# Optimization experiments

Hardware: AMD Instinct MI355X
Metric: run time of the kernel (lower is better)

Reference implementation:

```python
import jax, jax.numpy as jnp
import numpy as np

N = 4096       # num nodes
E = 131072     # num edges (avg degree 32)
IN = 128       # in_channels
H = 256        # hidden_channels
NC = 16        # num_classes
NH = 4         # num_heads
HD = H // NH   # head dim
EPS = 1e-5


def setup_inputs() -> dict:
    key = jax.random.key(0)
    ks = jax.random.split(key, 16)
    p = lambda k, sh, s=0.05: jax.random.normal(k, sh, jnp.float32) * s
    return {
        "x": jax.random.normal(ks[0], (N, IN), jnp.float32),
        "edge_index": jax.random.randint(ks[1], (2, E), 0, N),
        "edge_attr": jax.random.uniform(ks[2], (E,), jnp.float32),
        # GCN layers
        "W_gcn1": p(ks[3], (IN, H)), "b_gcn1": jnp.zeros((H,), jnp.float32),
        "W_gcn2": p(ks[4], (H, H)), "b_gcn2": jnp.zeros((H,), jnp.float32),
        # Transformer encoder layer (post-norm, batch_first)
        "in_proj_w": p(ks[5], (3 * H, H)), "in_proj_b": jnp.zeros((3 * H,), jnp.float32),
        "out_proj_w": p(ks[6], (H, H)), "out_proj_b": jnp.zeros((H,), jnp.float32),
        "ln1_g": jnp.ones((H,), jnp.float32), "ln1_b": jnp.zeros((H,), jnp.float32),
        "ffn_w1": p(ks[7], (H, 4 * H)), "ffn_b1": jnp.zeros((4 * H,), jnp.float32),
        "ffn_w2": p(ks[8], (4 * H, H)), "ffn_b2": jnp.zeros((H,), jnp.float32),
        "ln2_g": jnp.ones((H,), jnp.float32), "ln2_b": jnp.zeros((H,), jnp.float32),
        # classifier head
        "W_cls": p(ks[9], (H, NC)), "b_cls": jnp.zeros((NC,), jnp.float32),
        # semantic decoder
        "W_d1": p(ks[10], (H, 2 * H)), "b_d1": jnp.zeros((2 * H,), jnp.float32),
        "W_d2": p(ks[11], (2 * H, 3)), "b_d2": jnp.zeros((3,), jnp.float32),
    }


def gcn_conv(x, edge_index, edge_weight, W, b):
    """PyG GCNConv: add self-loops, symmetric norm, gather-matmul-scatter."""
    n = x.shape[0]
    src, dst = edge_index[0], edge_index[1]
    loop = jnp.arange(n)
    src_f = jnp.concatenate([src, loop])
    dst_f = jnp.concatenate([dst, loop])
    ew_f = jnp.concatenate([edge_weight, jnp.ones((n,), x.dtype)])
    deg = jax.ops.segment_sum(ew_f, dst_f, num_segments=n)
    dinv = jnp.where(deg > 0, jax.lax.rsqrt(deg), 0.0)
    norm = dinv[src_f] * ew_f * dinv[dst_f]            # [E+N]
    h = x @ W                                          # [N,H]
    out = jax.ops.segment_sum(norm[:, None] * h[src_f], dst_f, num_segments=n)
    return out + b


def layer_norm(x, g, b):
    mu = jnp.mean(x, axis=-1, keepdims=True)
    var = jnp.mean(jnp.square(x - mu), axis=-1, keepdims=True)
    return (x - mu) * jax.lax.rsqrt(var + EPS) * g + b


def transformer_layer(x, in_proj_w, in_proj_b, out_proj_w, out_proj_b,
                      ln1_g, ln1_b, ffn_w1, ffn_b1, ffn_w2, ffn_b2, ln2_g, ln2_b):
    # Self-attention (seq = all N nodes, batch of 1), eval mode (no dropout)
    qkv = x @ in_proj_w.T + in_proj_b                  # [N,3H]
    q, k, v = jnp.split(qkv, 3, axis=-1)
    q = q.reshape(-1, NH, HD) * (1.0 / np.sqrt(HD))
    k = k.reshape(-1, NH, HD)
    v = v.reshape(-1, NH, HD)
    scores = jnp.einsum("nhd,mhd->hnm", q, k)          # [NH,N,N]
    attn = jax.nn.softmax(scores, axis=-1)
    ctx = jnp.einsum("hnm,mhd->nhd", attn, v).reshape(-1, H)
    attn_out = ctx @ out_proj_w.T + out_proj_b
    x = layer_norm(x + attn_out, ln1_g, ln1_b)         # post-norm
    ffn = jax.nn.relu(x @ ffn_w1 + ffn_b1) @ ffn_w2 + ffn_b2
    return layer_norm(x + ffn, ln2_g, ln2_b)


def reference(x, edge_index, edge_attr,
              W_gcn1, b_gcn1, W_gcn2, b_gcn2,
              in_proj_w, in_proj_b, out_proj_w, out_proj_b,
              ln1_g, ln1_b, ffn_w1, ffn_b1, ffn_w2, ffn_b2, ln2_g, ln2_b,
              W_cls, b_cls, W_d1, b_d1, W_d2, b_d2):
    x_local = jax.nn.relu(gcn_conv(x, edge_index, edge_attr, W_gcn1, b_gcn1))
    # F.dropout with training=False is identity
    x_local = gcn_conv(x_local, edge_index, edge_attr, W_gcn2, b_gcn2)
    x_global = transformer_layer(x_local, in_proj_w, in_proj_b, out_proj_w,
                                 out_proj_b, ln1_g, ln1_b, ffn_w1, ffn_b1,
                                 ffn_w2, ffn_b2, ln2_g, ln2_b)
    x_final = x_local + x_global
    out_cls = jax.nn.log_softmax(x_final @ W_cls + b_cls, axis=1)
    out_reco = jax.nn.sigmoid(jax.nn.relu(x_final @ W_d1 + b_d1) @ W_d2 + b_d2)
    return (out_cls, out_reco)
```

## Files before the change

### kernel.cpp

```cpp
#include <hip/hip_runtime.h>
#include <hip/hip_bf16.h>

#define N_NODES 4096
#define N_EDGES 131072
#define KSPLIT 8

typedef short bf16x8 __attribute__((ext_vector_type(8)));
typedef float f32x4  __attribute__((ext_vector_type(4)));

#if __has_builtin(__builtin_amdgcn_exp2f)
#define EXP2F __builtin_amdgcn_exp2f
#else
#define EXP2F exp2f
#endif

#define QSCL 0.1803368801111743f

static __device__ __forceinline__ float b2f(__hip_bfloat16 x) { return __bfloat162float(x); }
static __device__ __forceinline__ __hip_bfloat16 f2b(float x) { return __float2bfloat16(x); }
static __device__ __forceinline__ short f2bs(float x) {
    __hip_bfloat16 h = __float2bfloat16(x);
    return *reinterpret_cast<short*>(&h);
}
static __device__ __forceinline__ float us2f(ushort u) {
    union { unsigned i; float f; } x; x.i = ((unsigned)u) << 16; return x.f;
}
static __device__ __forceinline__ unsigned pack2(float lo, float hi) {
    return (unsigned)(ushort)f2bs(lo) | ((unsigned)(ushort)f2bs(hi) << 16);
}

static __device__ __forceinline__ float rmax16(float v) {
    v = fmaxf(v, __shfl_xor(v, 1));
    v = fmaxf(v, __shfl_xor(v, 2));
    v = fmaxf(v, __shfl_xor(v, 4));
    v = fmaxf(v, __shfl_xor(v, 8));
    return v;
}
static __device__ __forceinline__ float rsum16(float v) {
    v += __shfl_xor(v, 1);
    v += __shfl_xor(v, 2);
    v += __shfl_xor(v, 4);
    v += __shfl_xor(v, 8);
    return v;
}
static __device__ __forceinline__ int is_f32(const unsigned* ln1g_raw) {
    return ln1g_raw[0] == 0x3F800000u ? 1 : 0;
}
static __device__ __forceinline__ int is_i64(const unsigned* ei_raw) {
    unsigned acc = 0;
#pragma unroll
    for (int j = 1; j < 32; j += 2) acc |= ei_raw[j];
    return acc == 0u ? 1 : 0;
}

struct Ptrs24 { const void* p[24]; };

#define CAST_TOTAL 1681171

__global__ __launch_bounds__(256) void cast_all(Ptrs24 ptrs, const unsigned* __restrict__ ln1g_raw,
                                                __hip_bfloat16* __restrict__ canon) {
    const int sizes[24] = {524288,131072,32768,256,65536,256,196608,768,65536,256,
                           256,256,262144,1024,262144,256,256,256,4096,16,
                           131072,512,1536,3};
    const long i0 = ((long)blockIdx.x * 256 + threadIdx.x) * 8;
    if (i0 >= CAST_TOTAL) return;
    const int f32 = is_f32(ln1g_raw);
    int off = (int)i0, seg = 0, base = 0;
    bool done = false;
#pragma unroll
    for (int s = 0; s < 24; s++) {
        if (!done) {
            if (off < sizes[s]) { seg = s; done = true; }
            else { off -= sizes[s]; base += sizes[s]; }
        }
    }
    const void* p = ptrs.p[seg];
    ushort ov[8];
    int Rlog = -1, C = 0;
    if (seg == 2)       { Rlog = 7;  C = 256; }
    else if (seg == 4)  { Rlog = 8;  C = 256; }
    else if (seg == 12) { Rlog = 8;  C = 1024; }
    else if (seg == 14) { Rlog = 10; C = 256; }
    else if (seg == 20) { Rlog = 8;  C = 512; }
    if (Rlog >= 0) {
        const int c = off >> Rlog;
        const int k0 = off & ((1 << Rlog) - 1);
#pragma unroll
        for (int j = 0; j < 8; j++) {
            const int src = (k0 + j) * C + c;
            float v = f32 ? ((const float*)p)[src] : us2f(((const ushort*)p)[src]);
            ov[j] = (ushort)f2bs(v);
        }
    } else if (off + 8 > sizes[seg]) {
        for (int j = 0; j < 8; j++) {
            if (off + j < sizes[seg]) {
                float v = f32 ? ((const float*)p)[off + j] : us2f(((const ushort*)p)[off + j]);
                canon[base + off + j] = f2b(v);
            }
        }
        return;
    } else if (f32) {
        uint4 a = *(const uint4*)((const float*)p + off);
        uint4 b = *(const uint4*)((const float*)p + off + 4);
        const float* fa = (const float*)&a;
        const float* fb = (const float*)&b;
#pragma unroll
        for (int j = 0; j < 4; j++) { ov[j] = (ushort)f2bs(fa[j]); ov[4 + j] = (ushort)f2bs(fb[j]); }
    } else {
        uint4 a = *(const uint4*)((const ushort*)p + off);
        *(uint4*)ov = a;
    }
    *(uint4*)((ushort*)canon + base + off) = *(uint4*)ov;
}

static __device__ __forceinline__ int ld_idx(const void* ei, int k, int i64) {
    return i64 ? (int)((const long long*)ei)[k] : ((const int*)ei)[k];
}

__global__ __launch_bounds__(256) void deg_init_k(float* deg, int* cnt) {
    int i = blockIdx.x * 256 + threadIdx.x;
    if (i < N_NODES) { deg[i] = 1.0f; cnt[i] = 0; }
}

__global__ __launch_bounds__(256) void deg_scat_k(const void* __restrict__ ei,
                                                  const __hip_bfloat16* __restrict__ ew,
                                                  float* deg, int* cnt) {
    const int i64 = is_i64((const unsigned*)ei);
    int e = blockIdx.x * 256 + threadIdx.x;
    if (e < N_EDGES) {
        int d = ld_idx(ei, N_EDGES + e, i64);
        atomicAdd(&deg[d], b2f(ew[e]));
        atomicAdd(&cnt[d], 1);
    }
}

__global__ __launch_bounds__(256) void scan_k(const float* __restrict__ deg, float* dinv,
                                              int* cnt, int* rowptr) {
    __shared__ int ss[256];
    const int t = threadIdx.x;
    const int base = t * 16;
    int loc[16];
    int run = 0;
#pragma unroll
    for (int j = 0; j < 16; j++) { loc[j] = run; run += cnt[base + j]; }
    ss[t] = run;
    __syncthreads();
    for (int off = 1; off < 256; off <<= 1) {
        int v = (t >= off) ? ss[t - off] : 0;
        __syncthreads();
        ss[t] += v;
        __syncthreads();
    }
    int pre = (t == 0) ? 0 : ss[t - 1];
#pragma unroll
    for (int j = 0; j < 16; j++) rowptr[base + j] = pre + loc[j];
    if (t == 255) rowptr[N_NODES] = pre + run;
    for (int i = t; i < N_NODES; i += 256) {
        float dg = deg[i];
        dinv[i] = dg > 0.f ? rsqrtf(dg) : 0.f;
        cnt[i] = 0;
    }
}

__global__ __launch_bounds__(256) void fill_k(const void* __restrict__ ei,
                                              const __hip_bfloat16* __restrict__ ew,
                                              const float* __restrict__ dinv,
                                              const int* __restrict__ rowptr,
                                              int* cur, int* csrc, float* cw) {
    const int i64 = is_i64((const unsigned*)ei);
    int e = blockIdx.x * 256 + threadIdx.x;
    if (e < N_EDGES) {
        int s = ld_idx(ei, e, i64), d = ld_idx(ei, N_EDGES + e, i64);
        int p = atomicAdd(&cur[d], 1);
        int slot = rowptr[d] + p;
// ... 21 lines not shown
        ushort4 bv  = *(const ushort4*)((const ushort*)bias + c0);
        const float dii = di * di;
        acc[0] = fmaf(dii, us2f(own.x), us2f(bv.x));
        acc[1] = fmaf(dii, us2f(own.y), us2f(bv.y));
        acc[2] = fmaf(dii, us2f(own.z), us2f(bv.z));
        acc[3] = fmaf(dii, us2f(own.w), us2f(bv.w));
    }
    int p = rowptr[n];
    const int end = rowptr[n + 1];
    for (; p + 4 <= end; p += 4) {
        int s0 = csrc[p], s1 = csrc[p + 1], s2 = csrc[p + 2], s3 = csrc[p + 3];
        float w0 = cw[p], w1 = cw[p + 1], w2 = cw[p + 2], w3 = cw[p + 3];
        ushort4 v0 = *(const ushort4*)(hp + (size_t)s0 * 256 + c0);
        ushort4 v1 = *(const ushort4*)(hp + (size_t)s1 * 256 + c0);
        ushort4 v2 = *(const ushort4*)(hp + (size_t)s2 * 256 + c0);
        ushort4 v3 = *(const ushort4*)(hp + (size_t)s3 * 256 + c0);
        acc[0] = fmaf(w0, us2f(v0.x), acc[0]); acc[1] = fmaf(w0, us2f(v0.y), acc[1]);
        acc[2] = fmaf(w0, us2f(v0.z), acc[2]); acc[3] = fmaf(w0, us2f(v0.w), acc[3]);
        acc[0] = fmaf(w1, us2f(v1.x), acc[0]); acc[1] = fmaf(w1, us2f(v1.y), acc[1]);
        acc[2] = fmaf(w1, us2f(v1.z), acc[2]); acc[3] = fmaf(w1, us2f(v1.w), acc[3]);
        acc[0] = fmaf(w2, us2f(v2.x), acc[0]); acc[1] = fmaf(w2, us2f(v2.y), acc[1]);
        acc[2] = fmaf(w2, us2f(v2.z), acc[2]); acc[3] = fmaf(w2, us2f(v2.w), acc[3]);
        acc[0] = fmaf(w3, us2f(v3.x), acc[0]); acc[1] = fmaf(w3, us2f(v3.y), acc[1]);
        acc[2] = fmaf(w3, us2f(v3.z), acc[2]); acc[3] = fmaf(w3, us2f(v3.w), acc[3]);
    }
    for (; p < end; p++) {
        int s = csrc[p];
        float wgt = cw[p];
        ushort4 v = *(const ushort4*)(hp + (size_t)s * 256 + c0);
        acc[0] = fmaf(wgt, us2f(v.x), acc[0]); acc[1] = fmaf(wgt, us2f(v.y), acc[1]);
        acc[2] = fmaf(wgt, us2f(v.z), acc[2]); acc[3] = fmaf(wgt, us2f(v.w), acc[3]);
    }
    if (RELU) {
#pragma unroll
        for (int j = 0; j < 4; j++) acc[j] = fmaxf(acc[j], 0.f);
    }
    ushort4 o;
    o.x = (ushort)f2bs(acc[0]); o.y = (ushort)f2bs(acc[1]);
    o.z = (ushort)f2bs(acc[2]); o.w = (ushort)f2bs(acc[3]);
    *(ushort4*)((ushort*)out + (size_t)n * 256 + c0) = o;
}

template <bool BIAS, bool RELU>
__global__ __launch_bounds__(256) void gemm64(const __hip_bfloat16* __restrict__ A,
                                              const __hip_bfloat16* __restrict__ Bt,
                                              const __hip_bfloat16* __restrict__ bias,
                                              __hip_bfloat16* __restrict__ C,
                                              int K, int Nn) {
    __shared__ __align__(16) short As[64 * 72];
    __shared__ __align__(16) short Bs[64 * 72];
    const int t = threadIdx.x;
    const int m0 = blockIdx.y * 64, n0 = blockIdx.x * 64;
    const int lane = t & 63, w = t >> 6, li = lane & 15, quad = lane >> 4;

    f32x4 acc[4];
#pragma unroll
    for (int i = 0; i < 4; i++) acc[i] = (f32x4){0.f, 0.f, 0.f, 0.f};

    for (int k0 = 0; k0 < K; k0 += 64) {
#pragma unroll
        for (int i = 0; i < 2; i++) {
            int idx = i * 256 + t;
            int r = idx >> 3, c8 = (idx & 7) * 8;
            uint4 va = *(const uint4*)((const ushort*)A + (size_t)(m0 + r) * K + k0 + c8);
            *(uint4*)&As[r * 72 + c8] = va;
            uint4 vb = *(const uint4*)((const ushort*)Bt + (size_t)(n0 + r) * K + k0 + c8);
            *(uint4*)&Bs[r * 72 + c8] = vb;
        }
        __syncthreads();
#pragma unroll
        for (int kk = 0; kk < 64; kk += 32) {
            bf16x8 a = *(const bf16x8*)&As[(w * 16 + li) * 72 + kk + quad * 8];
#pragma unroll
            for (int nt = 0; nt < 4; nt++) {
                bf16x8 b = *(const bf16x8*)&Bs[(nt * 16 + li) * 72 + kk + quad * 8];
                acc[nt] = __builtin_amdgcn_mfma_f32_16x16x32_bf16(a, b, acc[nt], 0, 0, 0);
            }
        }
        __syncthreads();
    }
#pragma unroll
    for (int nt = 0; nt < 4; nt++) {
        const int col = n0 + nt * 16 + li;
        const float bv = BIAS ? b2f(bias[col]) : 0.f;
#pragma unroll
        for (int r = 0; r < 4; r++) {
            const int row = m0 + w * 16 + quad * 4 + r;
            float v = acc[nt][r] + bv;
            if (RELU) v = fmaxf(v, 0.f);
            C[(size_t)row * Nn + col] = f2b(v);
        }
    }
}

template <bool BIAS, bool RELU>
__global__ __launch_bounds__(256) void gemm128(const __hip_bfloat16* __restrict__ A,
                                               const __hip_bfloat16* __restrict__ Bt,
                                               const __hip_bfloat16* __restrict__ bias,
                                               __hip_bfloat16* __restrict__ C,
                                               int K, int Nn) {
    __shared__ __align__(16) short As[128 * 72];
    __shared__ __align__(16) short Bs[128 * 72];
    const int t = threadIdx.x;
    const int m0 = blockIdx.y * 128, n0 = blockIdx.x * 128;
    const int lane = t & 63, w = t >> 6, li = lane & 15, quad = lane >> 4;
    const int wr = (w >> 1) * 64, wc = (w & 1) * 64;

    f32x4 acc[16];
#pragma unroll
    for (int i = 0; i < 16; i++) acc[i] = (f32x4){0.f, 0.f, 0.f, 0.f};

    for (int k0 = 0; k0 < K; k0 += 64) {
#pragma unroll
        for (int i = 0; i < 4; i++) {
            int idx = i * 256 + t;
            int r = idx >> 3, c8 = (idx & 7) * 8;
            uint4 va = *(const uint4*)((const ushort*)A + (size_t)(m0 + r) * K + k0 + c8);
            *(uint4*)&As[r * 72 + c8] = va;
            uint4 vb = *(const uint4*)((const ushort*)Bt + (size_t)(n0 + r) * K + k0 + c8);
            *(uint4*)&Bs[r * 72 + c8] = vb;
        }
        __syncthreads();
#pragma unroll
        for (int kk = 0; kk < 64; kk += 32) {
            bf16x8 a[4], b[4];
#pragma unroll
            for (int i = 0; i < 4; i++) {
                a[i] = *(const bf16x8*)&As[(wr + i * 16 + li) * 72 + kk + quad * 8];
                b[i] = *(const bf16x8*)&Bs[(wc + i * 16 + li) * 72 + kk + quad * 8];
            }
#pragma unroll
            for (int am = 0; am < 4; am++)
#pragma unroll
                for (int bn = 0; bn < 4; bn++)
                    acc[am * 4 + bn] = __builtin_amdgcn_mfma_f32_16x16x32_bf16(a[am], b[bn], acc[am * 4 + bn], 0, 0, 0);
        }
        __syncthreads();
    }
#pragma unroll
    for (int am = 0; am < 4; am++)
#pragma unroll
        for (int bn = 0; bn < 4; bn++) {
            const int col = n0 + wc + bn * 16 + li;
            const float bv = BIAS ? b2f(bias[col]) : 0.f;
#pragma unroll
            for (int r = 0; r < 4; r++) {
                const int row = m0 + wr + am * 16 + quad * 4 + r;
                float v = acc[am * 4 + bn][r] + bv;
                if (RELU) v = fmaxf(v, 0.f);
                C[(size_t)row * Nn + col] = f2b(v);
            }
        }
}

__global__ __launch_bounds__(256) void attn_part(const __hip_bfloat16* __restrict__ qkv,
                                                 __hip_bfloat16* __restrict__ Opart,
                                                 float* __restrict__ Lpart) {
    __shared__ __align__(16) short Ks[64 * 72];
    __shared__ __align__(16) short Vt[64 * 72];
    const int t = threadIdx.x;
    const int h = blockIdx.y;
    const int q0 = blockIdx.x * 64;
    const int kz = blockIdx.z;
    const int lane = t & 63, w = t >> 6, li = lane & 15, quad = lane >> 4;
    const ushort* qp = (const ushort*)qkv;

    const int kr0 = t >> 3, kd0 = (t & 7) * 8;
    const int jbeg = kz * (N_NODES / KSPLIT);
    const int jend = jbeg + N_NODES / KSPLIT;

    uint4 kreg0 = *(const uint4*)(qp + (size_t)(jbeg + kr0) * 768 + 256 + h * 64 + kd0);
    uint4 kreg1 = *(const uint4*)(qp + (size_t)(jbeg + 32 + kr0) * 768 + 256 + h * 64 + kd0);
    uint4 vreg0 = *(const uint4*)(qp + (size_t)(jbeg + lane) * 768 + 512 + h * 64 + w * 8);
    uint4 vreg1 = *(const uint4*)(qp + (size_t)(jbeg + lane) * 768 + 512 + h * 64 + (4 + w) * 8);

// ... 59 lines not shown
            for (int r = 0; r < 4; r++) {
                float p = EXP2F(T[nt][r]);
                T[nt][r] = p;
                rs += p;
            }
        rs += __shfl_xor(rs, 16);
        rs += __shfl_xor(rs, 32);
        l_run += rs;

        unsigned pd[4][2];
#pragma unroll
        for (int nt = 0; nt < 4; nt++) {
            pd[nt][0] = pack2(T[nt][0], T[nt][1]);
            pd[nt][1] = pack2(T[nt][2], T[nt][3]);
        }

#pragma unroll
        for (int c = 0; c < 2; c++) {
            const int tl = 2 * c, th = 2 * c + 1;
            unsigned aL0 = (unsigned)__shfl((int)pd[tl][0], srcA);
            unsigned aL1 = (unsigned)__shfl((int)pd[tl][1], srcA);
            unsigned aH0 = (unsigned)__shfl((int)pd[th][0], srcA);
            unsigned aH1 = (unsigned)__shfl((int)pd[th][1], srcA);
            unsigned bL0 = (unsigned)__shfl((int)pd[tl][0], srcB);
            unsigned bL1 = (unsigned)__shfl((int)pd[tl][1], srcB);
            unsigned bH0 = (unsigned)__shfl((int)pd[th][0], srcB);
            unsigned bH1 = (unsigned)__shfl((int)pd[th][1], srcB);
            unsigned af[4];
            af[0] = hi_t ? aH0 : aL0;
            af[1] = hi_t ? aH1 : aL1;
            af[2] = hi_t ? bH0 : bL0;
            af[3] = hi_t ? bH1 : bL1;
            bf16x8 afrag = *(const bf16x8*)af;
#pragma unroll
            for (int nt2 = 0; nt2 < 4; nt2++) {
                bf16x8 vf = *(const bf16x8*)&Vt[(nt2 * 16 + li) * 72 + c * 32 + quad * 8];
                O[nt2] = __builtin_amdgcn_mfma_f32_16x16x32_bf16(afrag, vf, O[nt2], 0, 0, 0);
            }
        }
        __syncthreads();
    }

    const int hb = kz * 4 + h;
    ushort* ob = (ushort*)Opart + ((size_t)hb * 4096 + q0) * 64;
#pragma unroll
    for (int nt = 0; nt < 4; nt++)
#pragma unroll
        for (int r = 0; r < 4; r++)
            ob[(size_t)(w * 16 + quad * 4 + r) * 64 + nt * 16 + li] = (ushort)f2bs(O[nt][r]);
    if (quad == 0)
        Lpart[(size_t)hb * 4096 + q0 + w * 16 + li] = l_run;
}

template <bool COMB, bool ADDAFTER>
__global__ __launch_bounds__(256) void gemm_ln(const __hip_bfloat16* __restrict__ Asrc,
                                               const float* __restrict__ Lpart,
                                               const __hip_bfloat16* __restrict__ Bt,
                                               const __hip_bfloat16* __restrict__ bias,
                                               const __hip_bfloat16* __restrict__ res,
                                               const __hip_bfloat16* __restrict__ gw,
                                               const __hip_bfloat16* __restrict__ bw,
                                               const __hip_bfloat16* __restrict__ addsrc,
                                               __hip_bfloat16* __restrict__ out, int K) {
    __shared__ __align__(16) short As[16 * 72];
    __shared__ __align__(16) short Bs[256 * 72];
    __shared__ float redS[4][16];
    __shared__ float redQ[4][16];
    const int t = threadIdx.x;
    const int m0 = blockIdx.x * 16;
    const int lane = t & 63, w = t >> 6, li = lane & 15, quad = lane >> 4;
    const ushort* Ap = (const ushort*)Asrc;
    const ushort* Bp = (const ushort*)Bt;
    const int NIT = K >> 6;

    f32x4 acc[4];
#pragma unroll
    for (int i = 0; i < 4; i++) acc[i] = (f32x4){0.f, 0.f, 0.f, 0.f};

    const int bn = t >> 3, bk0 = (t & 7) * 8;
    const int ar = t >> 3, ak0 = (t & 7) * 8;

    uint4 breg[8];
    uint4 areg;
#pragma unroll
    for (int it2 = 0; it2 < 8; it2++)
        breg[it2] = *(const uint4*)(Bp + (size_t)(it2 * 32 + bn) * K + bk0);
    if (!COMB && t < 128)
        areg = *(const uint4*)(Ap + (size_t)(m0 + ar) * K + ak0);

    for (int kb = 0; kb < NIT; kb++) {
#pragma unroll
        for (int it2 = 0; it2 < 8; it2++)
            *(uint4*)&Bs[(it2 * 32 + bn) * 72 + bk0] = breg[it2];
        if (COMB) {
            if (t < 128) {
                const int hd = kb;
                const int row = m0 + ar;
                float L = 0.f;
#pragma unroll
                for (int s = 0; s < KSPLIT; s++) L += Lpart[(size_t)(s * 4 + hd) * 4096 + row];
                const float inv = 1.f / L;
                float sum[8] = {0.f,0.f,0.f,0.f,0.f,0.f,0.f,0.f};
#pragma unroll
                for (int s = 0; s < KSPLIT; s++) {
                    uint4 v = *(const uint4*)(Ap + ((size_t)(s * 4 + hd) * 4096 + row) * 64 + ak0);
                    const ushort* sv = (const ushort*)&v;
#pragma unroll
                    for (int j = 0; j < 8; j++) sum[j] += us2f(sv[j]);
                }
                ushort ov[8];
#pragma unroll
                for (int j = 0; j < 8; j++) ov[j] = (ushort)f2bs(sum[j] * inv);
                *(uint4*)&As[ar * 72 + ak0] = *(uint4*)ov;
            }
        } else if (t < 128) {
            *(uint4*)&As[ar * 72 + ak0] = areg;
        }
        __syncthreads();
        if (kb + 1 < NIT) {
            const int kbase = (kb + 1) * 64;
#pragma unroll
            for (int it2 = 0; it2 < 8; it2++)
                breg[it2] = *(const uint4*)(Bp + (size_t)(it2 * 32 + bn) * K + kbase + bk0);
            if (!COMB && t < 128)
                areg = *(const uint4*)(Ap + (size_t)(m0 + ar) * K + kbase + ak0);
        }
#pragma unroll
        for (int kk = 0; kk < 64; kk += 32) {
            bf16x8 a = *(const bf16x8*)&As[li * 72 + kk + quad * 8];
#pragma unroll
            for (int nt = 0; nt < 4; nt++) {
                bf16x8 b = *(const bf16x8*)&Bs[(w * 64 + nt * 16 + li) * 72 + kk + quad * 8];
                acc[nt] = __builtin_amdgcn_mfma_f32_16x16x32_bf16(a, b, acc[nt], 0, 0, 0);
            }
        }
        __syncthreads();
    }

    float x[4][4];
    float sx[4] = {0.f,0.f,0.f,0.f}, sq[4] = {0.f,0.f,0.f,0.f};
#pragma unroll
    for (int nt = 0; nt < 4; nt++) {
        const int col = w * 64 + nt * 16 + li;
        const float bv = b2f(bias[col]);
#pragma unroll
        for (int r = 0; r < 4; r++) {
            const int row = m0 + quad * 4 + r;
            float v = acc[nt][r] + bv + b2f(res[(size_t)row * 256 + col]);
            x[nt][r] = v;
            sx[r] += v;
            sq[r] += v * v;
        }
    }
#pragma unroll
    for (int r = 0; r < 4; r++) { sx[r] = rsum16(sx[r]); sq[r] = rsum16(sq[r]); }
    if (li == 0) {
#pragma unroll
        for (int r = 0; r < 4; r++) { redS[w][quad * 4 + r] = sx[r]; redQ[w][quad * 4 + r] = sq[r]; }
    }
    __syncthreads();
    float mu[4], rstd[4];
#pragma unroll
    for (int r = 0; r < 4; r++) {
        const int rl = quad * 4 + r;
        float S = redS[0][rl] + redS[1][rl] + redS[2][rl] + redS[3][rl];
        float Q = redQ[0][rl] + redQ[1][rl] + redQ[2][rl] + redQ[3][rl];
        float m = S * (1.f / 256.f);
        float var = Q * (1.f / 256.f) - m * m;
        mu[r] = m;
        rstd[r] = rsqrtf(var + 1e-5f);
    }
#pragma unroll
    for (int nt = 0; nt < 4; nt++) {
        const int col = w * 64 + nt * 16 + li;
        const float gv = b2f(gw[col]), bv2 = b2f(bw[col]);
#pragma unroll
        for (int r = 0; r < 4; r++) {
            const int row = m0 + quad * 4 + r;
            float y = (x[nt][r] - mu[r]) * rstd[r] * gv + bv2;
            if (ADDAFTER) y += b2f(addsrc[(size_t)row * 256 + col]);
            out[(size_t)row * 256 + col] = f2b(y);
        }
    }
}

__global__ __launch_bounds__(256) void gemm_reco(const __hip_bfloat16* __restrict__ xf,
                                                 const __hip_bfloat16* __restrict__ Bt,
                                                 const __hip_bfloat16* __restrict__ bd1,
                                                 const __hip_bfloat16* __restrict__ Wd2,
                                                 const __hip_bfloat16* __restrict__ bd2,
                                                 const unsigned* __restrict__ ln1g_raw,
                                                 void* __restrict__ out) {
    __shared__ __align__(16) short As[16 * 40];
    __shared__ __align__(16) short Bs[512 * 40];
    __shared__ float W2s[512 * 3];
    __shared__ float red[4][16][3];
    const int t = threadIdx.x;
    const int m0 = blockIdx.x * 16;
    const int lane = t & 63, w = t >> 6, li = lane & 15, quad = lane >> 4;
    const ushort* Ap = (const ushort*)xf;
    const ushort* Bp = (const ushort*)Bt;
    const int K = 256;

    for (int i = t; i < 1536; i += 256) W2s[i] = b2f(Wd2[i]);

    f32x4 acc[8];
#pragma unroll
    for (int i = 0; i < 8; i++) acc[i] = (f32x4){0.f, 0.f, 0.f, 0.f};

    const int bn = t >> 2, bk0 = (t & 3) * 8;
    const int ar = t >> 2, ak0 = (t & 3) * 8;

    uint4 breg[8];
    uint4 areg;
#pragma unroll
    for (int it2 = 0; it2 < 8; it2++)
        breg[it2] = *(const uint4*)(Bp + (size_t)(it2 * 64 + bn) * K + bk0);
    if (t < 64) areg = *(const uint4*)(Ap + (size_t)(m0 + ar) * K + ak0);

    for (int kb = 0; kb < 8; kb++) {
#pragma unroll
        for (int it2 = 0; it2 < 8; it2++)
            *(uint4*)&Bs[(it2 * 64 + bn) * 40 + bk0] = breg[it2];
        if (t < 64) *(uint4*)&As[ar * 40 + ak0] = areg;
        __syncthreads();
        if (kb + 1 < 8) {
            const int kbase = (kb + 1) * 32;
#pragma unroll
            for (int it2 = 0; it2 < 8; it2++)
                breg[it2] = *(const uint4*)(Bp + (size_t)(it2 * 64 + bn) * K + kbase + bk0);
            if (t < 64) areg = *(const uint4*)(Ap + (size_t)(m0 + ar) * K + kbase + ak0);
        }
        bf16x8 a = *(const bf16x8*)&As[li * 40 + quad * 8];
#pragma unroll
        for (int nt = 0; nt < 8; nt++) {
            bf16x8 b = *(const bf16x8*)&Bs[(w * 128 + nt * 16 + li) * 40 + quad * 8];
            acc[nt] = __builtin_amdgcn_mfma_f32_16x16x32_bf16(a, b, acc[nt], 0, 0, 0);
        }
        __syncthreads();
    }

    float p3[3][4];
#pragma unroll
    for (int c = 0; c < 3; c++)
#pragma unroll
        for (int r = 0; r < 4; r++) p3[c][r] = 0.f;
#pragma unroll
    for (int nt = 0; nt < 8; nt++) {
        const int col = w * 128 + nt * 16 + li;
        const float bv = b2f(bd1[col]);
        const float w0 = W2s[col * 3 + 0], w1 = W2s[col * 3 + 1], w2 = W2s[col * 3 + 2];
#pragma unroll
        for (int r = 0; r < 4; r++) {
            float hv = fmaxf(acc[nt][r] + bv, 0.f);
            p3[0][r] = fmaf(hv, w0, p3[0][r]);
            p3[1][r] = fmaf(hv, w1, p3[1][r]);
            p3[2][r] = fmaf(hv, w2, p3[2][r]);
        }
    }
#pragma unroll
    for (int c = 0; c < 3; c++)
#pragma unroll
        for (int r = 0; r < 4; r++) {
            float s = rsum16(p3[c][r]);
            if (li == 0) red[w][quad * 4 + r][c] = s;
        }
    __syncthreads();
    if (t < 48) {
        const int rl = t / 3, c = t % 3;
        float s = red[0][rl][c] + red[1][rl][c] + red[2][rl][c] + red[3][rl][c] + b2f(bd2[c]);
        float v = 1.f / (1.f + __expf(-s));
        const size_t oidx = (size_t)(N_NODES * 16) + (size_t)(m0 + rl) * 3 + c;
        if (is_f32(ln1g_raw)) ((float*)out)[oidx] = v;
        else                  ((__hip_bfloat16*)out)[oidx] = f2b(v);
    }
}

__global__ __launch_bounds__(256) void cls16(const __hip_bfloat16* __restrict__ xf,
                                             const __hip_bfloat16* __restrict__ W,
                                             const __hip_bfloat16* __restrict__ b,
                                             const unsigned* __restrict__ ln1g_raw,
                                             void* __restrict__ out) {
    __shared__ float Ws[256 * 16];
    __shared__ float bs[16];
    const int t = threadIdx.x;
    for (int i = t; i < 4096; i += 256) Ws[i] = b2f(W[i]);
    if (t < 16) bs[t] = b2f(b[t]);
    __syncthreads();
    const int c = t & 15, rl = t >> 4;
    const int row = blockIdx.x * 16 + rl;
    const ushort* xr = (const ushort*)xf + (size_t)row * 256;
    float acc = bs[c];
    for (int k0 = 0; k0 < 256; k0 += 8) {
        uint4 v = *(const uint4*)(xr + k0);
        const ushort* sv = (const ushort*)&v;
#pragma unroll
        for (int j = 0; j < 8; j++) acc = fmaf(us2f(sv[j]), Ws[(k0 + j) * 16 + c], acc);
    }
    float mx = rmax16(acc);
    float se = rsum16(__expf(acc - mx));
    float v = acc - mx - __logf(se);
    const size_t oidx = (size_t)row * 16 + c;
    if (is_f32(ln1g_raw)) ((float*)out)[oidx] = v;
    else                  ((__hip_bfloat16*)out)[oidx] = f2b(v);
}

extern "C" void kernel_launch(void* const* d_in, const int* in_sizes, int n_in,
                              void* d_out, int out_size, void* d_ws, size_t ws_size,
                              hipStream_t stream) {
    char* ws = (char*)d_ws;
    __hip_bfloat16* canon = (__hip_bfloat16*)(ws + 256);
    float* deg    = (float*)(ws + 3362816);
    int*   cnt    = (int*)  (ws + 3379200);
    int*   rowptr = (int*)  (ws + 3395584);
    float* dinv   = (float*)(ws + 3412224);
    int*   csrc   = (int*)  (ws + 3428608);
    float* cw     = (float*)(ws + 3952896);
    __hip_bfloat16* h     = (__hip_bfloat16*)(ws + 4477184);
    __hip_bfloat16* x1    = (__hip_bfloat16*)(ws + 6574336);
    __hip_bfloat16* xloc  = (__hip_bfloat16*)(ws + 8671488);
    __hip_bfloat16* big   = (__hip_bfloat16*)(ws + 10768640);
    __hip_bfloat16* y1    = (__hip_bfloat16*)(ws + 23351552);
    __hip_bfloat16* xfin  = (__hip_bfloat16*)(ws + 25448704);
    __hip_bfloat16* Opart = (__hip_bfloat16*)(ws + 27545856);
    float* Lpart = (float*)(ws + 6574336);

    const __hip_bfloat16* xc    = canon + 0;
    const __hip_bfloat16* eac   = canon + 524288;
    const __hip_bfloat16* Wg1   = canon + 655360;
    const __hip_bfloat16* bg1   = canon + 688128;
    const __hip_bfloat16* Wg2   = canon + 688384;
    const __hip_bfloat16* bg2   = canon + 753920;
    const __hip_bfloat16* ipw   = canon + 754176;
    const __hip_bfloat16* ipb   = canon + 950784;
    const __hip_bfloat16* opw   = canon + 951552;
    const __hip_bfloat16* opb   = canon + 1017088;
    const __hip_bfloat16* ln1g  = canon + 1017344;
    const __hip_bfloat16* ln1b  = canon + 1017600;
    const __hip_bfloat16* fw1   = canon + 1017856;
    const __hip_bfloat16* fb1   = canon + 1280000;
    const __hip_bfloat16* fw2   = canon + 1281024;
    const __hip_bfloat16* fb2   = canon + 1543168;
    const __hip_bfloat16* ln2g  = canon + 1543424;
    const __hip_bfloat16* ln2b  = canon + 1543680;
    const __hip_bfloat16* Wcls  = canon + 1543936;
    const __hip_bfloat16* bcls  = canon + 1548032;
    const __hip_bfloat16* Wd1   = canon + 1548048;
    const __hip_bfloat16* bd1   = canon + 1679120;
    const __hip_bfloat16* Wd2   = canon + 1679632;
    const __hip_bfloat16* bd2   = canon + 1681168;

    const void* ei = d_in[1];
    const unsigned* ln1g_raw = (const unsigned*)d_in[11];

    Ptrs24 pt;
    {
        const int map[24] = {0,2,3,4,5,6,7,8,9,10,11,12,13,14,15,16,17,18,19,20,21,22,23,24};
        for (int i = 0; i < 24; i++) pt.p[i] = d_in[map[i]];
    }

    const dim3 b256(256);

    deg_init_k<<<16, b256, 0, stream>>>(deg, cnt);
    cast_all<<<(CAST_TOTAL / 8 + 256) / 256, b256, 0, stream>>>(pt, ln1g_raw, canon);

    deg_scat_k<<<512, b256, 0, stream>>>(ei, eac, deg, cnt);
    scan_k<<<1, b256, 0, stream>>>(deg, dinv, cnt, rowptr);
    fill_k<<<512, b256, 0, stream>>>(ei, eac, dinv, rowptr, cnt, csrc, cw);

    gemm64<false, false><<<dim3(4, 64), b256, 0, stream>>>(xc, Wg1, nullptr, h, 128, 256);
    gcn_agg<true><<<1024, b256, 0, stream>>>(h, dinv, rowptr, csrc, cw, bg1, x1);
    gemm64<false, false><<<dim3(4, 64), b256, 0, stream>>>(x1, Wg2, nullptr, h, 256, 256);
    gcn_agg<false><<<1024, b256, 0, stream>>>(h, dinv, rowptr, csrc, cw, bg2, xloc);

    gemm128<true, false><<<dim3(6, 32), b256, 0, stream>>>(xloc, ipw, ipb, big, 256, 768);
    attn_part<<<dim3(64, 4, KSPLIT), b256, 0, stream>>>(big, Opart, Lpart);
    gemm_ln<true, false><<<256, b256, 0, stream>>>(Opart, Lpart, opw, opb, xloc, ln1g, ln1b,
                                                   nullptr, y1, 256);
    gemm128<true, true><<<dim3(8, 32), b256, 0, stream>>>(y1, fw1, fb1, big, 256, 1024);
    gemm_ln<false, true><<<256, b256, 0, stream>>>(big, nullptr, fw2, fb2, y1, ln2g, ln2b,
                                                   xloc, xfin, 1024);

    cls16<<<256, b256, 0, stream>>>(xfin, Wcls, bcls, ln1g_raw, d_out);
    gemm_reco<<<256, b256, 0, stream>>>(xfin, Wd1, bd1, Wd2, bd2, ln1g_raw, d_out);
}
```

Before: 332.4 us.

## Split fused GEMM+LayerNorm into tiled GEMMs plus row LN, prefetch GEMM tiles

Several unrelated changes land together. Each fused gemm_ln kernel (16-row tiles that reload the whole 256-column weight per block) becomes separate steps: attention-combine, a 64x64-tiled gemm64, then a per-row LayerNorm kernel. gemm64 and gemm128 now prefetch the next K tile into registers before the MFMA loop. deg init is folded into cast_all, and the cls and reco heads are merged into one launch. This trades more launches and extra global round-trips of intermediates for better GEMM parallelism and reuse.

```diff
diff --git a/kernel.cpp b/kernel.cpp
--- a/kernel.cpp
+++ b/kernel.cpp
@@ -58,11 +58,14 @@
 #define CAST_TOTAL 1681171
 
 __global__ __launch_bounds__(256) void cast_all(Ptrs24 ptrs, const unsigned* __restrict__ ln1g_raw,
-                                                __hip_bfloat16* __restrict__ canon) {
+                                                __hip_bfloat16* __restrict__ canon,
+                                                float* __restrict__ deg, int* __restrict__ cnt) {
+    const int gi = blockIdx.x * 256 + threadIdx.x;
+    if (gi < N_NODES) { deg[gi] = 1.0f; cnt[gi] = 0; }
     const int sizes[24] = {524288,131072,32768,256,65536,256,196608,768,65536,256,
                            256,256,262144,1024,262144,256,256,256,4096,16,
                            131072,512,1536,3};
-    const long i0 = ((long)blockIdx.x * 256 + threadIdx.x) * 8;
+    const long i0 = (long)gi * 8;
     if (i0 >= CAST_TOTAL) return;
     const int f32 = is_f32(ln1g_raw);
     int off = (int)i0, seg = 0, base = 0;
@@ -115,11 +118,6 @@
 
 static __device__ __forceinline__ int ld_idx(const void* ei, int k, int i64) {
     return i64 ? (int)((const long long*)ei)[k] : ((const int*)ei)[k];
-}
-
-__global__ __launch_bounds__(256) void deg_init_k(float* deg, int* cnt) {
-    int i = blockIdx.x * 256 + threadIdx.x;
-    if (i < N_NODES) { deg[i] = 1.0f; cnt[i] = 0; }
 }
 
 __global__ __launch_bounds__(256) void deg_scat_k(const void* __restrict__ ei,
@@ -247,22 +245,35 @@
     const int t = threadIdx.x;
     const int m0 = blockIdx.y * 64, n0 = blockIdx.x * 64;
     const int lane = t & 63, w = t >> 6, li = lane & 15, quad = lane >> 4;
+    const int sr = t >> 3, sc = (t & 7) * 8;
 
     f32x4 acc[4];
 #pragma unroll
     for (int i = 0; i < 4; i++) acc[i] = (f32x4){0.f, 0.f, 0.f, 0.f};
 
-    for (int k0 = 0; k0 < K; k0 += 64) {
+    uint4 pa[2], pb[2];
+#pragma unroll
+    for (int i = 0; i < 2; i++) {
+        pa[i] = *(const uint4*)((const ushort*)A + (size_t)(m0 + i * 32 + sr) * K + sc);
+        pb[i] = *(const uint4*)((const ushort*)Bt + (size_t)(n0 + i * 32 + sr) * K + sc);
+    }
+
+    const int NIT = K >> 6;
+    for (int kb = 0; kb < NIT; kb++) {
 #pragma unroll
         for (int i = 0; i < 2; i++) {
-            int idx = i * 256 + t;
-            int r = idx >> 3, c8 = (idx & 7) * 8;
-            uint4 va = *(const uint4*)((const ushort*)A + (size_t)(m0 + r) * K + k0 + c8);
-            *(uint4*)&As[r * 72 + c8] = va;
-            uint4 vb = *(const uint4*)((const ushort*)Bt + (size_t)(n0 + r) * K + k0 + c8);
-            *(uint4*)&Bs[r * 72 + c8] = vb;
-        }
-        __syncthreads();
+            *(uint4*)&As[(i * 32 + sr) * 72 + sc] = pa[i];
+            *(uint4*)&Bs[(i * 32 + sr) * 72 + sc] = pb[i];
+        }
+        __syncthreads();
+        if (kb + 1 < NIT) {
+            const int kbase = (kb + 1) * 64;
+#pragma unroll
+            for (int i = 0; i < 2; i++) {
+                pa[i] = *(const uint4*)((const ushort*)A + (size_t)(m0 + i * 32 + sr) * K + kbase + sc);
+                pb[i] = *(const uint4*)((const ushort*)Bt + (size_t)(n0 + i * 32 + sr) * K + kbase + sc);
+            }
+        }
 #pragma unroll
         for (int kk = 0; kk < 64; kk += 32) {
             bf16x8 a = *(const bf16x8*)&As[(w * 16 + li) * 72 + kk + quad * 8];
@@ -300,22 +311,35 @@
     const int m0 = blockIdx.y * 128, n0 = blockIdx.x * 128;
     const int lane = t & 63, w = t >> 6, li = lane & 15, quad = lane >> 4;
     const int wr = (w >> 1) * 64, wc = (w & 1) * 64;
+    const int sr = t >> 3, sc = (t & 7) * 8;
 
     f32x4 acc[16];
 #pragma unroll
     for (int i = 0; i < 16; i++) acc[i] = (f32x4){0.f, 0.f, 0.f, 0.f};
 
-    for (int k0 = 0; k0 < K; k0 += 64) {
+    uint4 pa[4], pb[4];
+#pragma unroll
+    for (int i = 0; i < 4; i++) {
+        pa[i] = *(const uint4*)((const ushort*)A + (size_t)(m0 + i * 32 + sr) * K + sc);
+        pb[i] = *(const uint4*)((const ushort*)Bt + (size_t)(n0 + i * 32 + sr) * K + sc);
+    }
+
+    const int NIT = K >> 6;
+    for (int kb = 0; kb < NIT; kb++) {
 #pragma unroll
         for (int i = 0; i < 4; i++) {
-            int idx = i * 256 + t;
-            int r = idx >> 3, c8 = (idx & 7) * 8;
-            uint4 va = *(const uint4*)((const ushort*)A + (size_t)(m0 + r) * K + k0 + c8);
-            *(uint4*)&As[r * 72 + c8] = va;
-            uint4 vb = *(const uint4*)((const ushort*)Bt + (size_t)(n0 + r) * K + k0 + c8);
-            *(uint4*)&Bs[r * 72 + c8] = vb;
-        }
-        __syncthreads();
+            *(uint4*)&As[(i * 32 + sr) * 72 + sc] = pa[i];
+            *(uint4*)&Bs[(i * 32 + sr) * 72 + sc] = pb[i];
+        }
+        __syncthreads();
+        if (kb + 1 < NIT) {
+            const int kbase = (kb + 1) * 64;
+#pragma unroll
+            for (int i = 0; i < 4; i++) {
+                pa[i] = *(const uint4*)((const ushort*)A + (size_t)(m0 + i * 32 + sr) * K + kbase + sc);
+                pb[i] = *(const uint4*)((const ushort*)Bt + (size_t)(n0 + i * 32 + sr) * K + kbase + sc);
+            }
+        }
 #pragma unroll
         for (int kk = 0; kk < 64; kk += 32) {
             bf16x8 a[4], b[4];
@@ -481,257 +505,188 @@
         Lpart[(size_t)hb * 4096 + q0 + w * 16 + li] = l_run;
 }
 
-template <bool COMB, bool ADDAFTER>
-__global__ __launch_bounds__(256) void gemm_ln(const __hip_bfloat16* __restrict__ Asrc,
-                                               const float* __restrict__ Lpart,
-                                               const __hip_bfloat16* __restrict__ Bt,
-                                               const __hip_bfloat16* __restrict__ bias,
-                                               const __hip_bfloat16* __restrict__ res,
-                                               const __hip_bfloat16* __restrict__ gw,
-                                               const __hip_bfloat16* __restrict__ bw,
-                                               const __hip_bfloat16* __restrict__ addsrc,
-                                               __hip_bfloat16* __restrict__ out, int K) {
-    __shared__ __align__(16) short As[16 * 72];
-    __shared__ __align__(16) short Bs[256 * 72];
-    __shared__ float redS[4][16];
-    __shared__ float redQ[4][16];
+__global__ __launch_bounds__(256) void attn_comb(const __hip_bfloat16* __restrict__ Opart,
+                                                 const float* __restrict__ Lpart,
+                                                 __hip_bfloat16* __restrict__ ctx) {
     const int t = threadIdx.x;
-    const int m0 = blockIdx.x * 16;
-    const int lane = t & 63, w = t >> 6, li = lane & 15, quad = lane >> 4;
-    const ushort* Ap = (const ushort*)Asrc;
-    const ushort* Bp = (const ushort*)Bt;
-    const int NIT = K >> 6;
-
-    f32x4 acc[4];
-#pragma unroll
-    for (int i = 0; i < 4; i++) acc[i] = (f32x4){0.f, 0.f, 0.f, 0.f};
-
-    const int bn = t >> 3, bk0 = (t & 7) * 8;
-    const int ar = t >> 3, ak0 = (t & 7) * 8;
-
-    uint4 breg[8];
-    uint4 areg;
-#pragma unroll
-    for (int it2 = 0; it2 < 8; it2++)
-        breg[it2] = *(const uint4*)(Bp + (size_t)(it2 * 32 + bn) * K + bk0);
-    if (!COMB && t < 128)
-        areg = *(const uint4*)(Ap + (size_t)(m0 + ar) * K + ak0);
-
-    for (int kb = 0; kb < NIT; kb++) {
-#pragma unroll
-        for (int it2 = 0; it2 < 8; it2++)
-            *(uint4*)&Bs[(it2 * 32 + bn) * 72 + bk0] = breg[it2];
-        if (COMB) {
-            if (t < 128) {
-                const int hd = kb;
-                const int row = m0 + ar;
-                float L = 0.f;
-#pragma unroll
-                for (int s = 0; s < KSPLIT; s++) L += Lpart[(size_t)(s * 4 + hd) * 4096 + row];
-                const float inv = 1.f / L;
-                float sum[8] = {0.f,0.f,0.f,0.f,0.f,0.f,0.f,0.f};
-#pragma unroll
-                for (int s = 0; s < KSPLIT; s++) {
-                    uint4 v = *(const uint4*)(Ap + ((size_t)(s * 4 + hd) * 4096 + row) * 64 + ak0);
-                    const ushort* sv = (const ushort*)&v;
-#pragma unroll
-                    for (int j = 0; j < 8; j++) sum[j] += us2f(sv[j]);
-                }
-                ushort ov[8];
-#pragma unroll
-                for (int j = 0; j < 8; j++) ov[j] = (ushort)f2bs(sum[j] * inv);
-                *(uint4*)&As[ar * 72 + ak0] = *(uint4*)ov;
-            }
-        } else if (t < 128) {
-            *(uint4*)&As[ar * 72 + ak0] = areg;
-        }
-        __syncthreads();
-        if (kb + 1 < NIT) {
-            const int kbase = (kb + 1) * 64;
-#pragma unroll
-            for (int it2 = 0; it2 < 8; it2++)
-                breg[it2] = *(const uint4*)(Bp + (size_t)(it2 * 32 + bn) * K + kbase + bk0);
-            if (!COMB && t < 128)
-                areg = *(const uint4*)(Ap + (size_t)(m0 + ar) * K + kbase + ak0);
-        }
-#pragma unroll
-        for (int kk = 0; kk < 64; kk += 32) {
-            bf16x8 a = *(const bf16x8*)&As[li * 72 + kk + quad * 8];
-#pragma unroll
-            for (int nt = 0; nt < 4; nt++) {
-                bf16x8 b = *(const bf16x8*)&Bs[(w * 64 + nt * 16 + li) * 72 + kk + quad * 8];
-                acc[nt] = __builtin_amdgcn_mfma_f32_16x16x32_bf16(a, b, acc[nt], 0, 0, 0);
-            }
-        }
-        __syncthreads();
-    }
-
-    float x[4][4];
-    float sx[4] = {0.f,0.f,0.f,0.f}, sq[4] = {0.f,0.f,0.f,0.f};
-#pragma unroll
-    for (int nt = 0; nt < 4; nt++) {
-        const int col = w * 64 + nt * 16 + li;
-        const float bv = b2f(bias[col]);
-#pragma unroll
-        for (int r = 0; r < 4; r++) {
-            const int row = m0 + quad * 4 + r;
-            float v = acc[nt][r] + bv + b2f(res[(size_t)row * 256 + col]);
-            x[nt][r] = v;
-            sx[r] += v;
-            sq[r] += v * v;
-        }
-    }
-#pragma unroll
-    for (int r = 0; r < 4; r++) { sx[r] = rsum16(sx[r]); sq[r] = rsum16(sq[r]); }
-    if (li == 0) {
-#pragma unroll
-        for (int r = 0; r < 4; r++) { redS[w][quad * 4 + r] = sx[r]; redQ[w][quad * 4 + r] = sq[r]; }
-    }
+    const int h = blockIdx.y;
+    const int row = blockIdx.x * 64 + (t >> 2);
+    const int d0 = (t & 3) * 16;
+    float L = 0.f;
+#pragma unroll
+    for (int s = 0; s < KSPLIT; s++) L += Lpart[(size_t)(s * 4 + h) * 4096 + row];
+    const float inv = 1.f / L;
+    float o[16];
+#pragma unroll
+    for (int j = 0; j < 16; j++) o[j] = 0.f;
+#pragma unroll
+    for (int s = 0; s < KSPLIT; s++) {
+        const ushort* base = (const ushort*)Opart + ((size_t)(s * 4 + h) * 4096 + row) * 64 + d0;
+        uint4 v0 = *(const uint4*)base;
+        uint4 v1 = *(const uint4*)(base + 8);
+        const ushort* sv0 = (const ushort*)&v0;
+        const ushort* sv1 = (const ushort*)&v1;
+#pragma unroll
+        for (int j = 0; j < 8; j++) {
+            o[j]     += us2f(sv0[j]);
+            o[8 + j] += us2f(sv1[j]);
+        }
+    }
+    ushort pk[16];
+#pragma unroll
+    for (int j = 0; j < 16; j++) pk[j] = (ushort)f2bs(o[j] * inv);
+    ushort* dst = (ushort*)ctx + (size_t)row * 256 + h * 64 + d0;
+    *(uint4*)dst = *(uint4*)pk;
+    *(uint4*)(dst + 8) = *(uint4*)(pk + 8);
+}
+
+template <bool ADDC>
+__global__ __launch_bounds__(256) void ln256(const __hip_bfloat16* __restrict__ A,
+                                             const __hip_bfloat16* __restrict__ Bv,
+                                             const __hip_bfloat16* __restrict__ gw,
+                                             const __hip_bfloat16* __restrict__ bw,
+                                             const __hip_bfloat16* __restrict__ Cadd,
+                                             __hip_bfloat16* __restrict__ out) {
+    __shared__ float red[8];
+    const int row = blockIdx.x, c = threadIdx.x;
+    const size_t o = (size_t)row * 256 + c;
+    float x = b2f(A[o]) + b2f(Bv[o]);
+    float s = x;
+#pragma unroll
+    for (int m = 1; m < 64; m <<= 1) s += __shfl_xor(s, m);
+    const int wv = c >> 6;
+    if ((c & 63) == 0) red[wv] = s;
     __syncthreads();
-    float mu[4], rstd[4];
-#pragma unroll
-    for (int r = 0; r < 4; r++) {
-        const int rl = quad * 4 + r;
-        float S = redS[0][rl] + redS[1][rl] + redS[2][rl] + redS[3][rl];
-        float Q = redQ[0][rl] + redQ[1][rl] + redQ[2][rl] + redQ[3][rl];
-        float m = S * (1.f / 256.f);
-        float var = Q * (1.f / 256.f) - m * m;
-        mu[r] = m;
-        rstd[r] = rsqrtf(var + 1e-5f);
-    }
-#pragma unroll
-    for (int nt = 0; nt < 4; nt++) {
-        const int col = w * 64 + nt * 16 + li;
-        const float gv = b2f(gw[col]), bv2 = b2f(bw[col]);
-#pragma unroll
-        for (int r = 0; r < 4; r++) {
-            const int row = m0 + quad * 4 + r;
-            float y = (x[nt][r] - mu[r]) * rstd[r] * gv + bv2;
-            if (ADDAFTER) y += b2f(addsrc[(size_t)row * 256 + col]);
-            out[(size_t)row * 256 + col] = f2b(y);
-        }
-    }
-}
-
-__global__ __launch_bounds__(256) void gemm_reco(const __hip_bfloat16* __restrict__ xf,
-                                                 const __hip_bfloat16* __restrict__ Bt,
-                                                 const __hip_bfloat16* __restrict__ bd1,
-                                                 const __hip_bfloat16* __restrict__ Wd2,
-                                                 const __hip_bfloat16* __restrict__ bd2,
-                                                 const unsigned* __restrict__ ln1g_raw,
-                                                 void* __restrict__ out) {
-    __shared__ __align__(16) short As[16 * 40];
-    __shared__ __align__(16) short Bs[512 * 40];
-    __shared__ float W2s[512 * 3];
-    __shared__ float red[4][16][3];
+    float mu = (red[0] + red[1] + red[2] + red[3]) * (1.f / 256.f);
+    float d = x - mu;
+    float s2 = d * d;
+#pragma unroll
+    for (int m = 1; m < 64; m <<= 1) s2 += __shfl_xor(s2, m);
+    if ((c & 63) == 0) red[4 + wv] = s2;
+    __syncthreads();
+    float var = (red[4] + red[5] + red[6] + red[7]) * (1.f / 256.f);
+    float y = d * rsqrtf(var + 1e-5f) * b2f(gw[c]) + b2f(bw[c]);
+    if (ADDC) y += b2f(Cadd[o]);
+    out[o] = f2b(y);
+}
+
+__global__ __launch_bounds__(256) void cls_reco(const __hip_bfloat16* __restrict__ xf,
+                                                const __hip_bfloat16* __restrict__ Wcls,
+                                                const __hip_bfloat16* __restrict__ bcls,
+                                                const __hip_bfloat16* __restrict__ Wd1t,
+                                                const __hip_bfloat16* __restrict__ bd1,
+                                                const __hip_bfloat16* __restrict__ Wd2,
+                                                const __hip_bfloat16* __restrict__ bd2,
+                                                const unsigned* __restrict__ ln1g_raw,
+                                                void* __restrict__ out) {
+    __shared__ __align__(16) char smem[49408];
     const int t = threadIdx.x;
-    const int m0 = blockIdx.x * 16;
-    const int lane = t & 63, w = t >> 6, li = lane & 15, quad = lane >> 4;
-    const ushort* Ap = (const ushort*)xf;
-    const ushort* Bp = (const ushort*)Bt;
-    const int K = 256;
-
-    for (int i = t; i < 1536; i += 256) W2s[i] = b2f(Wd2[i]);
-
-    f32x4 acc[8];
-#pragma unroll
-    for (int i = 0; i < 8; i++) acc[i] = (f32x4){0.f, 0.f, 0.f, 0.f};
-
-    const int bn = t >> 2, bk0 = (t & 3) * 8;
-    const int ar = t >> 2, ak0 = (t & 3) * 8;
-
-    uint4 breg[8];
-    uint4 areg;
-#pragma unroll
-    for (int it2 = 0; it2 < 8; it2++)
-        breg[it2] = *(const uint4*)(Bp + (size_t)(it2 * 64 + bn) * K + bk0);
-    if (t < 64) areg = *(const uint4*)(Ap + (size_t)(m0 + ar) * K + ak0);
-
-    for (int kb = 0; kb < 8; kb++) {
-#pragma unroll
-        for (int it2 = 0; it2 < 8; it2++)
-            *(uint4*)&Bs[(it2 * 64 + bn) * 40 + bk0] = breg[it2];
-        if (t < 64) *(uint4*)&As[ar * 40 + ak0] = areg;
-        __syncthreads();
-        if (kb + 1 < 8) {
-            const int kbase = (kb + 1) * 32;
-#pragma unroll
-            for (int it2 = 0; it2 < 8; it2++)
-                breg[it2] = *(const uint4*)(Bp + (size_t)(it2 * 64 + bn) * K + kbase + bk0);
-            if (t < 64) areg = *(const uint4*)(Ap + (size_t)(m0 + ar) * K + kbase + ak0);
-        }
-        bf16x8 a = *(const bf16x8*)&As[li * 40 + quad * 8];
-#pragma unroll
-        for (int nt = 0; nt < 8; nt++) {
-            bf16x8 b = *(const bf16x8*)&Bs[(w * 128 + nt * 16 + li) * 40 + quad * 8];
-            acc[nt] = __builtin_amdgcn_mfma_f32_16x16x32_bf16(a, b, acc[nt], 0, 0, 0);
-        }
-        __syncthreads();
-    }
-
-    float p3[3][4];
-#pragma unroll
-    for (int c = 0; c < 3; c++)
-#pragma unroll
-        for (int r = 0; r < 4; r++) p3[c][r] = 0.f;
-#pragma unroll
-    for (int nt = 0; nt < 8; nt++) {
-        const int col = w * 128 + nt * 16 + li;
-        const float bv = b2f(bd1[col]);
-        const float w0 = W2s[col * 3 + 0], w1 = W2s[col * 3 + 1], w2 = W2s[col * 3 + 2];
-#pragma unroll
-        for (int r = 0; r < 4; r++) {
-            float hv = fmaxf(acc[nt][r] + bv, 0.f);
-            p3[0][r] = fmaf(hv, w0, p3[0][r]);
-            p3[1][r] = fmaf(hv, w1, p3[1][r]);
-            p3[2][r] = fmaf(hv, w2, p3[2][r]);
-        }
-    }
-#pragma unroll
-    for (int c = 0; c < 3; c++)
-#pragma unroll
-        for (int r = 0; r < 4; r++) {
-            float s = rsum16(p3[c][r]);
-            if (li == 0) red[w][quad * 4 + r][c] = s;
-        }
-    __syncthreads();
-    if (t < 48) {
-        const int rl = t / 3, c = t % 3;
-        float s = red[0][rl][c] + red[1][rl][c] + red[2][rl][c] + red[3][rl][c] + b2f(bd2[c]);
-        float v = 1.f / (1.f + __expf(-s));
-        const size_t oidx = (size_t)(N_NODES * 16) + (size_t)(m0 + rl) * 3 + c;
+    if (blockIdx.x < 256) {
+        float* Ws = (float*)smem;
+        float* bs = (float*)(smem + 16384);
+        for (int i = t; i < 4096; i += 256) Ws[i] = b2f(Wcls[i]);
+        if (t < 16) bs[t] = b2f(bcls[t]);
+        __syncthreads();
+        const int c = t & 15, rl = t >> 4;
+        const int row = blockIdx.x * 16 + rl;
+        const ushort* xr = (const ushort*)xf + (size_t)row * 256;
+        float acc = bs[c];
+        for (int k0 = 0; k0 < 256; k0 += 8) {
+            uint4 v = *(const uint4*)(xr + k0);
+            const ushort* sv = (const ushort*)&v;
+#pragma unroll
+            for (int j = 0; j < 8; j++) acc = fmaf(us2f(sv[j]), Ws[(k0 + j) * 16 + c], acc);
+        }
+        float mx = rmax16(acc);
+        float se = rsum16(__expf(acc - mx));
+        float v = acc - mx - __logf(se);
+        const size_t oidx = (size_t)row * 16 + c;
         if (is_f32(ln1g_raw)) ((float*)out)[oidx] = v;
         else                  ((__hip_bfloat16*)out)[oidx] = f2b(v);
-    }
-}
-
-__global__ __launch_bounds__(256) void cls16(const __hip_bfloat16* __restrict__ xf,
-                                             const __hip_bfloat16* __restrict__ W,
-                                             const __hip_bfloat16* __restrict__ b,
-                                             const unsigned* __restrict__ ln1g_raw,
-                                             void* __restrict__ out) {
-    __shared__ float Ws[256 * 16];
-    __shared__ float bs[16];
-    const int t = threadIdx.x;
-    for (int i = t; i < 4096; i += 256) Ws[i] = b2f(W[i]);
-    if (t < 16) bs[t] = b2f(b[t]);
-    __syncthreads();
-    const int c = t & 15, rl = t >> 4;
-    const int row = blockIdx.x * 16 + rl;
-    const ushort* xr = (const ushort*)xf + (size_t)row * 256;
-    float acc = bs[c];
-    for (int k0 = 0; k0 < 256; k0 += 8) {
-        uint4 v = *(const uint4*)(xr + k0);
-        const ushort* sv = (const ushort*)&v;
-#pragma unroll
-        for (int j = 0; j < 8; j++) acc = fmaf(us2f(sv[j]), Ws[(k0 + j) * 16 + c], acc);
-    }
-    float mx = rmax16(acc);
-    float se = rsum16(__expf(acc - mx));
-    float v = acc - mx - __logf(se);
-    const size_t oidx = (size_t)row * 16 + c;
-    if (is_f32(ln1g_raw)) ((float*)out)[oidx] = v;
-    else                  ((__hip_bfloat16*)out)[oidx] = f2b(v);
+    } else {
+        short* As = (short*)smem;
+        short* Bs = (short*)(smem + 1280);
+        float* W2s = (float*)(smem + 42240);
+        float (*red)[16][3] = (float (*)[16][3])(smem + 48384);
+        const int m0 = (blockIdx.x - 256) * 16;
+        const int lane = t & 63, w = t >> 6, li = lane & 15, quad = lane >> 4;
+        const ushort* Ap = (const ushort*)xf;
+        const ushort* Bp = (const ushort*)Wd1t;
+        const int K = 256;
+
+        for (int i = t; i < 1536; i += 256) W2s[i] = b2f(Wd2[i]);
+
+        f32x4 acc[8];
+#pragma unroll
+        for (int i = 0; i < 8; i++) acc[i] = (f32x4){0.f, 0.f, 0.f, 0.f};
+
+        const int bn = t >> 2, bk0 = (t & 3) * 8;
+        const int ar = t >> 2, ak0 = (t & 3) * 8;
+
+        uint4 breg[8];
+        uint4 areg;
+#pragma unroll
+        for (int it2 = 0; it2 < 8; it2++)
+            breg[it2] = *(const uint4*)(Bp + (size_t)(it2 * 64 + bn) * K + bk0);
+        if (t < 64) areg = *(const uint4*)(Ap + (size_t)(m0 + ar) * K + ak0);
+
+        for (int kb = 0; kb < 8; kb++) {
+#pragma unroll
+            for (int it2 = 0; it2 < 8; it2++)
+                *(uint4*)&Bs[(it2 * 64 + bn) * 40 + bk0] = breg[it2];
+            if (t < 64) *(uint4*)&As[ar * 40 + ak0] = areg;
+            __syncthreads();
+            if (kb + 1 < 8) {
+                const int kbase = (kb + 1) * 32;
+#pragma unroll
+                for (int it2 = 0; it2 < 8; it2++)
+                    breg[it2] = *(const uint4*)(Bp + (size_t)(it2 * 64 + bn) * K + kbase + bk0);
+                if (t < 64) areg = *(const uint4*)(Ap + (size_t)(m0 + ar) * K + kbase + ak0);
+            }
+            bf16x8 a = *(const bf16x8*)&As[li * 40 + quad * 8];
+#pragma unroll
+            for (int nt = 0; nt < 8; nt++) {
+                bf16x8 b = *(const bf16x8*)&Bs[(w * 128 + nt * 16 + li) * 40 + quad * 8];
+                acc[nt] = __builtin_amdgcn_mfma_f32_16x16x32_bf16(a, b, acc[nt], 0, 0, 0);
+            }
+            __syncthreads();
+        }
+
+        float p3[3][4];
+#pragma unroll
+        for (int c = 0; c < 3; c++)
+#pragma unroll
+            for (int r = 0; r < 4; r++) p3[c][r] = 0.f;
+#pragma unroll
+        for (int nt = 0; nt < 8; nt++) {
+            const int col = w * 128 + nt * 16 + li;
+            const float bv = b2f(bd1[col]);
+            const float w0 = W2s[col * 3 + 0], w1 = W2s[col * 3 + 1], w2 = W2s[col * 3 + 2];
+#pragma unroll
+            for (int r = 0; r < 4; r++) {
+                float hv = fmaxf(acc[nt][r] + bv, 0.f);
+                p3[0][r] = fmaf(hv, w0, p3[0][r]);
+                p3[1][r] = fmaf(hv, w1, p3[1][r]);
+                p3[2][r] = fmaf(hv, w2, p3[2][r]);
+            }
+        }
+#pragma unroll
+        for (int c = 0; c < 3; c++)
+#pragma unroll
+            for (int r = 0; r < 4; r++) {
+                float s = rsum16(p3[c][r]);
+                if (li == 0) red[w][quad * 4 + r][c] = s;
+            }
+        __syncthreads();
+        if (t < 48) {
+            const int rl = t / 3, c = t % 3;
+            float s = red[0][rl][c] + red[1][rl][c] + red[2][rl][c] + red[3][rl][c] + b2f(bd2[c]);
+            float v = 1.f / (1.f + __expf(-s));
+            const size_t oidx = (size_t)(N_NODES * 16) + (size_t)(m0 + rl) * 3 + c;
+            if (is_f32(ln1g_raw)) ((float*)out)[oidx] = v;
+            else                  ((__hip_bfloat16*)out)[oidx] = f2b(v);
+        }
+    }
 }
 
 extern "C" void kernel_launch(void* const* d_in, const int* in_sizes, int n_in,
@@ -749,6 +704,8 @@
     __hip_bfloat16* x1    = (__hip_bfloat16*)(ws + 6574336);
     __hip_bfloat16* xloc  = (__hip_bfloat16*)(ws + 8671488);
     __hip_bfloat16* big   = (__hip_bfloat16*)(ws + 10768640);
+    __hip_bfloat16* ctxp  = (__hip_bfloat16*)(ws + 19157248);
+    __hip_bfloat16* attno = (__hip_bfloat16*)(ws + 21254400);
     __hip_bfloat16* y1    = (__hip_bfloat16*)(ws + 23351552);
     __hip_bfloat16* xfin  = (__hip_bfloat16*)(ws + 25448704);
     __hip_bfloat16* Opart = (__hip_bfloat16*)(ws + 27545856);
@@ -790,8 +747,7 @@
 
     const dim3 b256(256);
 
-    deg_init_k<<<16, b256, 0, stream>>>(deg, cnt);
-    cast_all<<<(CAST_TOTAL / 8 + 256) / 256, b256, 0, stream>>>(pt, ln1g_raw, canon);
+    cast_all<<<(CAST_TOTAL / 8 + 256) / 256, b256, 0, stream>>>(pt, ln1g_raw, canon, deg, cnt);
 
     deg_scat_k<<<512, b256, 0, stream>>>(ei, eac, deg, cnt);
     scan_k<<<1, b256, 0, stream>>>(deg, dinv, cnt, rowptr);
@@ -804,12 +760,12 @@
 
     gemm128<true, false><<<dim3(6, 32), b256, 0, stream>>>(xloc, ipw, ipb, big, 256, 768);
     attn_part<<<dim3(64, 4, KSPLIT), b256, 0, stream>>>(big, Opart, Lpart);
-    gemm_ln<true, false><<<256, b256, 0, stream>>>(Opart, Lpart, opw, opb, xloc, ln1g, ln1b,
-                                                   nullptr, y1, 256);
+    attn_comb<<<dim3(64, 4), b256, 0, stream>>>(Opart, Lpart, ctxp);
+    gemm64<true, false><<<dim3(4, 64), b256, 0, stream>>>(ctxp, opw, opb, attno, 256, 256);
+    ln256<false><<<4096, b256, 0, stream>>>(xloc, attno, ln1g, ln1b, nullptr, y1);
     gemm128<true, true><<<dim3(8, 32), b256, 0, stream>>>(y1, fw1, fb1, big, 256, 1024);
-    gemm_ln<false, true><<<256, b256, 0, stream>>>(big, nullptr, fw2, fb2, y1, ln2g, ln2b,
-                                                   xloc, xfin, 1024);
-
-    cls16<<<256, b256, 0, stream>>>(xfin, Wcls, bcls, ln1g_raw, d_out);
-    gemm_reco<<<256, b256, 0, stream>>>(xfin, Wd1, bd1, Wd2, bd2, ln1g_raw, d_out);
-}
+    gemm64<true, false><<<dim3(4, 64), b256, 0, stream>>>(big, fw2, fb2, ctxp, 1024, 256);
+    ln256<true><<<4096, b256, 0, stream>>>(y1, ctxp, ln2g, ln2b, xloc, xfin);
+
+    cls_reco<<<512, b256, 0, stream>>>(xfin, Wcls, bcls, Wd1, bd1, Wd2, bd2, ln1g_raw, d_out);
+}
```

Measured after the change: 330.4 us. Within noise of the previous version (-0.6%).
